# Optimization experiments

Measured on AMD Instinct MI355X. Metric: run time of the kernel, lower is better.

## Reference

```python
import jax, jax.numpy as jnp
import numpy as np

WS = 8  # window_size
C_IN = 256
C_INNER = C_IN // 2  # default inner_channels = in_channels // 2
C_OUT = C_IN         # default out_channels = in_channels (needed for residual)


def setup_inputs() -> dict:
    key = jax.random.key(0)
    ks = jax.random.split(key, 9)
    B, C, T, H, W = 1, C_IN, 16, 128, 128
    x = jax.random.normal(ks[0], (B, C, T, H, W), dtype=jnp.float32)
    s = 0.02
    theta_w = jax.random.normal(ks[1], (C_INNER, C_IN), dtype=jnp.float32) * s
    theta_b = jnp.zeros((C_INNER,), dtype=jnp.float32)
    phi_w = jax.random.normal(ks[2], (C_INNER, C_IN), dtype=jnp.float32) * s
    phi_b = jnp.zeros((C_INNER,), dtype=jnp.float32)
    g_w = jax.random.normal(ks[3], (C_INNER, C_IN), dtype=jnp.float32) * s
    g_b = jnp.zeros((C_INNER,), dtype=jnp.float32)
    w_w = jax.random.normal(ks[4], (C_OUT, C_INNER), dtype=jnp.float32) * s
    w_b = jnp.zeros((C_OUT,), dtype=jnp.float32)
    return {"x": x, "theta_w": theta_w, "theta_b": theta_b,
            "phi_w": phi_w, "phi_b": phi_b, "g_w": g_w, "g_b": g_b,
            "w_w": w_w, "w_b": w_b}


def _window_partition(x, ws):
    # faithful to torch: view -> permute -> contiguous -> view(-1, C, ws, ws)
    B, C, T, H, W = x.shape
    x = x.reshape(B, C, T // ws, ws, H // ws, ws, W // ws, ws)
    x = jnp.transpose(x, (0, 1, 2, 4, 6, 3, 5, 7))
    return x.reshape(-1, C, ws, ws)


def _window_reverse(windows, ws, B, T, H, W):
    C = windows.shape[1]
    x = windows.reshape(B, C, T // ws, H // ws, W // ws, ws, ws, ws)
    x = jnp.transpose(x, (0, 1, 2, 5, 3, 6, 4, 7))
    return x.reshape(B, -1, T, H, W)


def _nonlocal_block(xw, theta_w, theta_b, phi_w, phi_b, g_w, g_b, w_w, w_b):
    # Embedded-Gaussian non-local block over each window; 1x1 convs = pointwise linear.
    N, C, h, w = xw.shape
    S = h * w  # positions within a window
    xf = xw.reshape(N, C, S)                                   # (N, C, S)
    theta = jnp.einsum('ic,ncs->nsi', theta_w, xf) + theta_b   # (N, S, inner)
    phi = jnp.einsum('ic,ncs->nis', phi_w, xf) + phi_b[:, None]  # (N, inner, S)
    g = jnp.einsum('ic,ncs->nsi', g_w, xf) + g_b               # (N, S, inner)
    f = jnp.einsum('nsi,nit->nst', theta, phi)                 # (N, S, S)
    attn = jax.nn.softmax(f, axis=-1)
    y = jnp.einsum('nst,nti->nsi', attn, g)                    # (N, S, inner)
    z = jnp.einsum('oi,nsi->nos', w_w, y) + w_b[:, None]       # (N, C_out, S)
    return z.reshape(N, -1, h, w) + xw                         # residual


def reference(x, theta_w, theta_b, phi_w, phi_b, g_w, g_b, w_w, w_b):
    B, C, T, H, W = x.shape
    xw = _window_partition(x, WS)
    aw = _nonlocal_block(xw, theta_w, theta_b, phi_w, phi_b, g_w, g_b, w_w, w_b)
    return _window_reverse(aw, WS, B, T, H, W)
```

## Files before the change

### kernel.cpp

```cpp
#include <hip/hip_runtime.h>

typedef float f32x4 __attribute__((ext_vector_type(4)));
typedef __bf16 bf16x8 __attribute__((ext_vector_type(8)));
typedef unsigned short u16x8 __attribute__((ext_vector_type(8)));

#define MFMA16x16x32 __builtin_amdgcn_mfma_f32_16x16x32_bf16

__device__ __forceinline__ unsigned short f2bf(float f) {
  union { float f; unsigned u; } v; v.f = f;
  unsigned r = v.u + 0x7fffu + ((v.u >> 16) & 1u);
  return (unsigned short)(r >> 16);
}
__device__ __forceinline__ float bf2f(unsigned short b) {
  union { unsigned u; float f; } v; v.u = ((unsigned)b) << 16;
  return v.f;
}
__device__ __forceinline__ bf16x8 ldb8(const unsigned short* p) {
  const u16x8* vp = (const u16x8*)__builtin_assume_aligned((const void*)p, 16);
  return __builtin_bit_cast(bf16x8, *vp);
}

__device__ __forceinline__ int sw8i(int idx) { return idx ^ (((idx >> 8) & 7) << 3); }
__device__ __forceinline__ int sw7i(int idx) { return idx ^ (((idx >> 7) & 7) << 3); }
__device__ __forceinline__ int sw6i(int idx) { return idx ^ (((idx >> 6) & 7) << 3); }

template <bool PRE>
__device__ __forceinline__ bf16x8 ldw(const unsigned short* q, const float* f, int off) {
  if constexpr (PRE) {
    return ldb8(q + off);
  } else {
    u16x8 u;
#pragma unroll
    for (int j = 0; j < 8; ++j) u[j] = f2bf(f[off + j]);
    return __builtin_bit_cast(bf16x8, u);
  }
}

__global__ void cvt_weights(const float* __restrict__ a, const float* __restrict__ b,
                            const float* __restrict__ c, const float* __restrict__ d,
                            unsigned short* __restrict__ o) {
  int i = blockIdx.x * 256 + threadIdx.x;
  int m = i >> 15, r = i & 32767;
  const float* s = (m == 0) ? a : (m == 1) ? b : (m == 2) ? c : d;
  o[i] = f2bf(s[r]);
}

template <bool PRE>
__global__ __launch_bounds__(256, 2) void nlb(
    const float* __restrict__ x, const unsigned short* __restrict__ wq,
    const float* __restrict__ tw, const float* __restrict__ pw,
    const float* __restrict__ gw, const float* __restrict__ wwp,
    const float* __restrict__ tbv, const float* __restrict__ pbv,
    const float* __restrict__ gbv, const float* __restrict__ wbv,
    float* __restrict__ out) {
  __shared__ __attribute__((aligned(16))) unsigned short Xbs[64 * 256];
  __shared__ __attribute__((aligned(16))) unsigned short Tht[64 * 128];
  __shared__ __attribute__((aligned(16))) unsigned short Pht[64 * 128];
  __shared__ __attribute__((aligned(16))) unsigned short Gs[128 * 64];

  const int tid = threadIdx.x;
  const int n = blockIdx.x;
  const int c = n >> 4;
  const int tb = (n >> 3) & 1;
  const int qq = n & 7;
  const int base = c * 262144 + tb * 131072 + qq * 2048;

  {
    const int s = tid & 63;
    const int sub = tid >> 6;
    const int h1 = sub >> 1;
    const int wh = s >> 3, ww = s & 7;
#pragma unroll
    for (int g = 0; g < 8; ++g) {
      const int wb = g * 2 + (sub & 1);
      const float* xp = x + base + h1 * 1024 + wh * 128 + wb * 8 + ww;
      u16x8 v;
#pragma unroll
      for (int wt = 0; wt < 8; ++wt) v[wt] = f2bf(xp[wt * 16384]);
      const int c0 = h1 * 128 + wb * 8;
      *(u16x8*)__builtin_assume_aligned((void*)&Xbs[sw8i(s * 256 + c0)], 16) = v;
    }
  }
  __syncthreads();

  const int lane = tid & 63;
  const int wv = tid >> 6;
  const int col = lane & 15;
  const int quad = lane >> 4;

  {
    f32x4 aT[2][4], aP[2][4], aG[2][4];
#pragma unroll
    for (int a = 0; a < 2; ++a)
#pragma unroll
      for (int b = 0; b < 4; ++b) { aT[a][b] = (f32x4)0.0f; aP[a][b] = (f32x4)0.0f; aG[a][b] = (f32x4)0.0f; }

#pragma unroll
    for (int ks = 0; ks < 8; ++ks) {
      const int k0 = ks * 32 + quad * 8;
      bf16x8 bfr[4];
#pragma unroll
      for (int nt = 0; nt < 4; ++nt)
        bfr[nt] = ldb8(&Xbs[sw8i((nt * 16 + col) * 256 + k0)]);
#pragma unroll
      for (int mtl = 0; mtl < 2; ++mtl) {
        const int m0 = wv * 32 + mtl * 16;
        const int aoff = (m0 + col) * 256 + k0;
        bf16x8 at = ldw<PRE>(wq + 0 * 32768, tw, aoff);
        bf16x8 ap = ldw<PRE>(wq + 1 * 32768, pw, aoff);
        bf16x8 ag = ldw<PRE>(wq + 2 * 32768, gw, aoff);
#pragma unroll
        for (int nt = 0; nt < 4; ++nt) {
          aT[mtl][nt] = MFMA16x16x32(at, bfr[nt], aT[mtl][nt], 0, 0, 0);
          aP[mtl][nt] = MFMA16x16x32(ap, bfr[nt], aP[mtl][nt], 0, 0, 0);
          aG[mtl][nt] = MFMA16x16x32(ag, bfr[nt], aG[mtl][nt], 0, 0, 0);
        }
      }
    }
#pragma unroll
    for (int mtl = 0; mtl < 2; ++mtl) {
      const int m0 = wv * 32 + mtl * 16;
#pragma unroll
      for (int r = 0; r < 4; ++r) {
        const int i = m0 + quad * 4 + r;
        const float bt = tbv[i], bp = pbv[i], bg = gbv[i];
#pragma unroll
        for (int nt = 0; nt < 4; ++nt) {
          const int s = nt * 16 + col;
          Tht[sw7i(s * 128 + i)] = f2bf(aT[mtl][nt][r] + bt);
          Pht[sw7i(s * 128 + i)] = f2bf(aP[mtl][nt][r] + bp);
          Gs[sw6i(i * 64 + s)] = f2bf(aG[mtl][nt][r] + bg);
        }
      }
    }
  }
  __syncthreads();

  unsigned short* At = Tht;
  {
    f32x4 accF[4];
#pragma unroll
    for (int b = 0; b < 4; ++b) accF[b] = (f32x4)0.0f;
    const int ms = wv * 16;
#pragma unroll
    for (int ks = 0; ks < 4; ++ks) {
      const int k0 = ks * 32 + quad * 8;
      bf16x8 af = ldb8(&Tht[sw7i((ms + col) * 128 + k0)]);
#pragma unroll
      for (int nt = 0; nt < 4; ++nt) {
        bf16x8 bp = ldb8(&Pht[sw7i((nt * 16 + col) * 128 + k0)]);
        accF[nt] = MFMA16x16x32(af, bp, accF[nt], 0, 0, 0);
      }
    }
    __syncthreads();

#pragma unroll
    for (int r = 0; r < 4; ++r) {
      float mx = fmaxf(fmaxf(accF[0][r], accF[1][r]), fmaxf(accF[2][r], accF[3][r]));
      mx = fmaxf(mx, __shfl_xor(mx, 1));
      mx = fmaxf(mx, __shfl_xor(mx, 2));
      mx = fmaxf(mx, __shfl_xor(mx, 4));
      mx = fmaxf(mx, __shfl_xor(mx, 8));
      float e0 = __expf(accF[0][r] - mx);
      float e1 = __expf(accF[1][r] - mx);
      float e2 = __expf(accF[2][r] - mx);
      float e3 = __expf(accF[3][r] - mx);
      float sum = e0 + e1 + e2 + e3;
      sum += __shfl_xor(sum, 1);
      sum += __shfl_xor(sum, 2);
      sum += __shfl_xor(sum, 4);
      sum += __shfl_xor(sum, 8);
      const float inv = 1.0f / sum;
      const int s = ms + quad * 4 + r;
      At[sw6i(s * 64 + 0 * 16 + col)] = f2bf(e0 * inv);
      At[sw6i(s * 64 + 1 * 16 + col)] = f2bf(e1 * inv);
      At[sw6i(s * 64 + 2 * 16 + col)] = f2bf(e2 * inv);
      At[sw6i(s * 64 + 3 * 16 + col)] = f2bf(e3 * inv);
    }
  }
  __syncthreads();

  unsigned short* Yt = Pht;
  {
    f32x4 accY[2][4];
#pragma unroll
    for (int a = 0; a < 2; ++a)
#pragma unroll
      for (int b = 0; b < 4; ++b) accY[a][b] = (f32x4)0.0f;
#pragma unroll
    for (int ks = 0; ks < 2; ++ks) {
      const int k0 = ks * 32 + quad * 8;
      bf16x8 bfr[4];
#pragma unroll
      for (int nt = 0; nt < 4; ++nt)
        bfr[nt] = ldb8(&At[sw6i((nt * 16 + col) * 64 + k0)]);
#pragma unroll
      for (int mtl = 0; mtl < 2; ++mtl) {
        const int m0 = wv * 32 + mtl * 16;
        bf16x8 ag = ldb8(&Gs[sw6i((m0 + col) * 64 + k0)]);
#pragma unroll
        for (int nt = 0; nt < 4; ++nt)
          accY[mtl][nt] = MFMA16x16x32(ag, bfr[nt], accY[mtl][nt], 0, 0, 0);
      }
    }
#pragma unroll
    for (int mtl = 0; mtl < 2; ++mtl) {
#pragma unroll
      for (int r = 0; r < 4; ++r) {
        const int i = wv * 32 + mtl * 16 + quad * 4 + r;
#pragma unroll
        for (int nt = 0; nt < 4; ++nt) {
          const int s = nt * 16 + col;
          Yt[sw7i(s * 128 + i)] = f2bf(accY[mtl][nt][r]);
        }
      }
    }
  }
  __syncthreads();

  {
    f32x4 accZ[4][4];
#pragma unroll
    for (int a = 0; a < 4; ++a)
#pragma unroll
      for (int b = 0; b < 4; ++b) accZ[a][b] = (f32x4)0.0f;
#pragma unroll
    for (int ks = 0; ks < 4; ++ks) {
      const int k0 = ks * 32 + quad * 8;
      bf16x8 bfr[4];
#pragma unroll
      for (int nt = 0; nt < 4; ++nt)
        bfr[nt] = ldb8(&Yt[sw7i((nt * 16 + col) * 128 + k0)]);
#pragma unroll
      for (int mtl = 0; mtl < 4; ++mtl) {
        const int m0 = wv * 64 + mtl * 16;
        bf16x8 aw = ldw<PRE>(wq + 3 * 32768, wwp, (m0 + col) * 128 + k0);
#pragma unroll
        for (int nt = 0; nt < 4; ++nt)
          accZ[mtl][nt] = MFMA16x16x32(aw, bfr[nt], accZ[mtl][nt], 0, 0, 0);
      }
    }
#pragma unroll
    for (int mtl = 0; mtl < 4; ++mtl) {
#pragma unroll
      for (int r = 0; r < 4; ++r) {
        const int o = wv * 64 + mtl * 16 + quad * 4 + r;
        const float bo = wbv[o];
        const int h1 = o >> 7, wb = (o >> 3) & 15, wt = o & 7;
        const int obase = base + wt * 16384 + h1 * 1024 + wb * 8;
#pragma unroll
        for (int nt = 0; nt < 4; ++nt) {
          const int s = nt * 16 + col;
          const int wh = s >> 3, ww = s & 7;
          const float v = accZ[mtl][nt][r] + bo + bf2f(Xbs[sw8i(s * 256 + o)]);
          out[obase + wh * 128 + ww] = v;
        }
      }
    }
  }
}

extern "C" void kernel_launch(void* const* d_in, const int* in_sizes, int n_in,
                              void* d_out, int out_size, void* d_ws, size_t ws_size,
                              hipStream_t stream) {
  const float* x = (const float*)d_in[0];
  const float* tw = (const float*)d_in[1];
  const float* tb = (const float*)d_in[2];
  const float* pw = (const float*)d_in[3];
  const float* pb = (const float*)d_in[4];
  const float* gw = (const float*)d_in[5];
  const float* gb = (const float*)d_in[6];
  const float* ww = (const float*)d_in[7];
  const float* wb = (const float*)d_in[8];
  float* out = (float*)d_out;

  const bool pre = ws_size >= (size_t)(131072 * 2);
  if (pre) {
    unsigned short* wq = (unsigned short*)d_ws;
    cvt_weights<<<512, 256, 0, stream>>>(tw, pw, gw, ww, wq);
    nlb<true><<<4096, 256, 0, stream>>>(x, wq, tw, pw, gw, ww, tb, pb, gb, wb, out);
  } else {
    nlb<false><<<4096, 256, 0, stream>>>(x, nullptr, tw, pw, gw, ww, tb, pb, gb, wb, out);
  }
}
```

Measured before the change: 569.3 us.

## Stage input loads and output stores through LDS for coalesced vector access

The input gather now loads x with contiguous float4 global reads into a swizzled LDS scratch buffer, then transposes to the bf16 channel-major layout. The output is likewise written to LDS scratch in two halves and stored with coalesced float4 writes, replacing scattered scalar accesses. The shared arrays are merged into one buffer so the scratch can alias the Theta/Phi/G regions. This adds extra LDS traffic and several block-wide barriers in exchange for fully coalesced global memory access.

```diff
diff --git a/kernel.cpp b/kernel.cpp
--- a/kernel.cpp
+++ b/kernel.cpp
@@ -3,6 +3,7 @@
 typedef float f32x4 __attribute__((ext_vector_type(4)));
 typedef __bf16 bf16x8 __attribute__((ext_vector_type(8)));
 typedef unsigned short u16x8 __attribute__((ext_vector_type(8)));
+typedef unsigned short u16x4 __attribute__((ext_vector_type(4)));
 
 #define MFMA16x16x32 __builtin_amdgcn_mfma_f32_16x16x32_bf16
 
@@ -53,10 +54,13 @@
     const float* __restrict__ tbv, const float* __restrict__ pbv,
     const float* __restrict__ gbv, const float* __restrict__ wbv,
     float* __restrict__ out) {
-  __shared__ __attribute__((aligned(16))) unsigned short Xbs[64 * 256];
-  __shared__ __attribute__((aligned(16))) unsigned short Tht[64 * 128];
-  __shared__ __attribute__((aligned(16))) unsigned short Pht[64 * 128];
-  __shared__ __attribute__((aligned(16))) unsigned short Gs[128 * 64];
+  __shared__ __attribute__((aligned(16))) unsigned short SH[40960];
+  unsigned short* Xbs = SH;
+  unsigned short* Tht = SH + 16384;
+  unsigned short* Pht = SH + 24576;
+  unsigned short* Gs  = SH + 32768;
+  float* scr = (float*)(SH + 16384);
+  f32x4* scr4 = (f32x4*)scr;
 
   const int tid = threadIdx.x;
   const int n = blockIdx.x;
@@ -65,28 +69,47 @@
   const int qq = n & 7;
   const int base = c * 262144 + tb * 131072 + qq * 2048;
 
-  {
-    const int s = tid & 63;
-    const int sub = tid >> 6;
-    const int h1 = sub >> 1;
-    const int wh = s >> 3, ww = s & 7;
-#pragma unroll
-    for (int g = 0; g < 8; ++g) {
-      const int wb = g * 2 + (sub & 1);
-      const float* xp = x + base + h1 * 1024 + wh * 128 + wb * 8 + ww;
-      u16x8 v;
-#pragma unroll
-      for (int wt = 0; wt < 8; ++wt) v[wt] = f2bf(xp[wt * 16384]);
-      const int c0 = h1 * 128 + wb * 8;
-      *(u16x8*)__builtin_assume_aligned((void*)&Xbs[sw8i(s * 256 + c0)], 16) = v;
-    }
-  }
-  __syncthreads();
-
   const int lane = tid & 63;
   const int wv = tid >> 6;
   const int col = lane & 15;
   const int quad = lane >> 4;
+
+  {
+    f32x4 ra[8], rb[8];
+#pragma unroll
+    for (int j = 0; j < 8; ++j) {
+      const int g4 = j * 256 + tid;
+      const int wt = g4 >> 9;
+      const int off = (g4 * 4) & 2047;
+      ra[j] = *(const f32x4*)(x + base + wt * 16384 + off);
+      rb[j] = *(const f32x4*)(x + base + (4 + wt) * 16384 + off);
+    }
+    const int wh = lane >> 3, ww = lane & 7;
+    const int h1 = wv >> 1;
+    const int wbp = wv & 1;
+#pragma unroll
+    for (int half = 0; half < 2; ++half) {
+#pragma unroll
+      for (int j = 0; j < 8; ++j) {
+        const int g4 = j * 256 + tid;
+        const int hl7 = (g4 >> 5) & 7;
+        scr4[g4 ^ hl7] = (half == 0) ? ra[j] : rb[j];
+      }
+      __syncthreads();
+#pragma unroll
+      for (int g = 0; g < 8; ++g) {
+        const int wb = g * 2 + wbp;
+        const int rbase = (h1 * 8 + wh) * 128 + wb * 8 + ww;
+        u16x4 v;
+#pragma unroll
+        for (int wt = 0; wt < 4; ++wt)
+          v[wt] = f2bf(scr[(wt * 2048 + rbase) ^ (wh << 2)]);
+        *(u16x4*)__builtin_assume_aligned(
+            (void*)&Xbs[sw8i(lane * 256 + h1 * 128 + wb * 8 + half * 4)], 8) = v;
+      }
+      __syncthreads();
+    }
+  }
 
   {
     f32x4 aT[2][4], aP[2][4], aG[2][4];
@@ -240,22 +263,39 @@
           accZ[mtl][nt] = MFMA16x16x32(aw, bfr[nt], accZ[mtl][nt], 0, 0, 0);
       }
     }
-#pragma unroll
-    for (int mtl = 0; mtl < 4; ++mtl) {
-#pragma unroll
-      for (int r = 0; r < 4; ++r) {
-        const int o = wv * 64 + mtl * 16 + quad * 4 + r;
-        const float bo = wbv[o];
-        const int h1 = o >> 7, wb = (o >> 3) & 15, wt = o & 7;
-        const int obase = base + wt * 16384 + h1 * 1024 + wb * 8;
-#pragma unroll
-        for (int nt = 0; nt < 4; ++nt) {
-          const int s = nt * 16 + col;
-          const int wh = s >> 3, ww = s & 7;
-          const float v = accZ[mtl][nt][r] + bo + bf2f(Xbs[sw8i(s * 256 + o)]);
-          out[obase + wh * 128 + ww] = v;
+    __syncthreads();
+
+#pragma unroll
+    for (int ch = 0; ch < 2; ++ch) {
+      if ((quad & 1) == ch) {
+#pragma unroll
+        for (int mtl = 0; mtl < 4; ++mtl) {
+#pragma unroll
+          for (int r = 0; r < 4; ++r) {
+            const int o = wv * 64 + mtl * 16 + quad * 4 + r;
+            const float bo = wbv[o];
+            const int h1 = o >> 7, wb = (o >> 3) & 15;
+#pragma unroll
+            for (int nt = 0; nt < 4; ++nt) {
+              const int s = nt * 16 + col;
+              const int wh = s >> 3, ww = s & 7;
+              const int hl = h1 * 8 + wh;
+              const float v = accZ[mtl][nt][r] + bo + bf2f(Xbs[sw8i(s * 256 + o)]);
+              scr[(r * 2048 + hl * 128 + wb * 8 + ww) ^ ((hl & 7) << 2)] = v;
+            }
+          }
         }
       }
+      __syncthreads();
+#pragma unroll
+      for (int j = 0; j < 8; ++j) {
+        const int g4 = j * 256 + tid;
+        const int wt = g4 >> 9;
+        const int off = (g4 * 4) & 2047;
+        const int hl7 = (g4 >> 5) & 7;
+        *(f32x4*)(out + base + (ch * 4 + wt) * 16384 + off) = scr4[g4 ^ hl7];
+      }
+      if (ch == 0) __syncthreads();
     }
   }
 }
```

Measured after the change: 572.0 us. No clear change (+0.5%).

## Alias shared buffers and hold residual in registers to fit three blocks per CU

Applied to the files above, without the earlier changes.

Shared memory shrinks from 80KB to 48KB. Theta and Phi now overwrite the X buffer once the projections finish, and the residual X values each thread needs are copied into registers before the overwrite. Launch bounds go from 2 to 3 blocks per CU, and the manual bf16 rounding is replaced by the compiler's native cast. This adds an extra barrier and 32 residual registers, which under the tighter register budget could cause spills.

```diff
diff --git a/kernel.cpp b/kernel.cpp
--- a/kernel.cpp
+++ b/kernel.cpp
@@ -3,13 +3,13 @@
 typedef float f32x4 __attribute__((ext_vector_type(4)));
 typedef __bf16 bf16x8 __attribute__((ext_vector_type(8)));
 typedef unsigned short u16x8 __attribute__((ext_vector_type(8)));
+typedef unsigned short u16x4 __attribute__((ext_vector_type(4)));
 
 #define MFMA16x16x32 __builtin_amdgcn_mfma_f32_16x16x32_bf16
 
 __device__ __forceinline__ unsigned short f2bf(float f) {
-  union { float f; unsigned u; } v; v.f = f;
-  unsigned r = v.u + 0x7fffu + ((v.u >> 16) & 1u);
-  return (unsigned short)(r >> 16);
+  __bf16 h = (__bf16)f;
+  return __builtin_bit_cast(unsigned short, h);
 }
 __device__ __forceinline__ float bf2f(unsigned short b) {
   union { unsigned u; float f; } v; v.u = ((unsigned)b) << 16;
@@ -18,6 +18,9 @@
 __device__ __forceinline__ bf16x8 ldb8(const unsigned short* p) {
   const u16x8* vp = (const u16x8*)__builtin_assume_aligned((const void*)p, 16);
   return __builtin_bit_cast(bf16x8, *vp);
+}
+__device__ __forceinline__ u16x4 ldb4(const unsigned short* p) {
+  return *(const u16x4*)__builtin_assume_aligned((const void*)p, 8);
 }
 
 __device__ __forceinline__ int sw8i(int idx) { return idx ^ (((idx >> 8) & 7) << 3); }
@@ -46,17 +49,18 @@
 }
 
 template <bool PRE>
-__global__ __launch_bounds__(256, 2) void nlb(
+__global__ __launch_bounds__(256, 3) void nlb(
     const float* __restrict__ x, const unsigned short* __restrict__ wq,
     const float* __restrict__ tw, const float* __restrict__ pw,
     const float* __restrict__ gw, const float* __restrict__ wwp,
     const float* __restrict__ tbv, const float* __restrict__ pbv,
     const float* __restrict__ gbv, const float* __restrict__ wbv,
     float* __restrict__ out) {
-  __shared__ __attribute__((aligned(16))) unsigned short Xbs[64 * 256];
-  __shared__ __attribute__((aligned(16))) unsigned short Tht[64 * 128];
-  __shared__ __attribute__((aligned(16))) unsigned short Pht[64 * 128];
-  __shared__ __attribute__((aligned(16))) unsigned short Gs[128 * 64];
+  __shared__ __attribute__((aligned(16))) unsigned short SH[24576];
+  unsigned short* Xbs = SH;
+  unsigned short* Gs  = SH + 16384;
+  unsigned short* Tht = SH;
+  unsigned short* Pht = SH + 8192;
 
   const int tid = threadIdx.x;
   const int n = blockIdx.x;
@@ -65,6 +69,13 @@
   const int qq = n & 7;
   const int base = c * 262144 + tb * 131072 + qq * 2048;
 
+  const int lane = tid & 63;
+  const int wv = tid >> 6;
+  const int col = lane & 15;
+  const int quad = lane >> 4;
+
+  u16x4 res[4][4];
+
   {
     const int s = tid & 63;
     const int sub = tid >> 6;
@@ -82,11 +93,6 @@
     }
   }
   __syncthreads();
-
-  const int lane = tid & 63;
-  const int wv = tid >> 6;
-  const int col = lane & 15;
-  const int quad = lane >> 4;
 
   {
     f32x4 aT[2][4], aP[2][4], aG[2][4];
@@ -119,17 +125,35 @@
     }
 #pragma unroll
     for (int mtl = 0; mtl < 2; ++mtl) {
-      const int m0 = wv * 32 + mtl * 16;
 #pragma unroll
       for (int r = 0; r < 4; ++r) {
-        const int i = m0 + quad * 4 + r;
-        const float bt = tbv[i], bp = pbv[i], bg = gbv[i];
+        const int i = wv * 32 + mtl * 16 + quad * 4 + r;
+        const float bg = gbv[i];
+#pragma unroll
+        for (int nt = 0; nt < 4; ++nt) {
+          const int s = nt * 16 + col;
+          Gs[sw6i(i * 64 + s)] = f2bf(aG[mtl][nt][r] + bg);
+        }
+      }
+    }
+#pragma unroll
+    for (int mtl = 0; mtl < 4; ++mtl)
+#pragma unroll
+      for (int nt = 0; nt < 4; ++nt)
+        res[mtl][nt] =
+            ldb4(&Xbs[sw8i((nt * 16 + col) * 256 + wv * 64 + mtl * 16 + quad * 4)]);
+    __syncthreads();
+#pragma unroll
+    for (int mtl = 0; mtl < 2; ++mtl) {
+#pragma unroll
+      for (int r = 0; r < 4; ++r) {
+        const int i = wv * 32 + mtl * 16 + quad * 4 + r;
+        const float bt = tbv[i], bp = pbv[i];
 #pragma unroll
         for (int nt = 0; nt < 4; ++nt) {
           const int s = nt * 16 + col;
           Tht[sw7i(s * 128 + i)] = f2bf(aT[mtl][nt][r] + bt);
           Pht[sw7i(s * 128 + i)] = f2bf(aP[mtl][nt][r] + bp);
-          Gs[sw6i(i * 64 + s)] = f2bf(aG[mtl][nt][r] + bg);
         }
       }
     }
@@ -252,7 +276,7 @@
         for (int nt = 0; nt < 4; ++nt) {
           const int s = nt * 16 + col;
           const int wh = s >> 3, ww = s & 7;
-          const float v = accZ[mtl][nt][r] + bo + bf2f(Xbs[sw8i(s * 256 + o)]);
+          const float v = accZ[mtl][nt][r] + bo + bf2f(res[mtl][nt][r]);
           out[obase + wh * 128 + ww] = v;
         }
       }
```

Result: faster. 557.9 us (-2.0%).
